# Kernel optimization log

Measured on AMD Instinct MI355X. Metric: run time of the kernel, lower is better.

The kernel has to match this reference:

```python
import jax, jax.numpy as jnp
import numpy as np

B, N, E, F = 8, 16384, 64, 64


def euler_zyx_to_matrix(J):
    # J: [..., 3] euler angles (alpha about Z, beta about Y, gamma about X)
    # R = Rz(alpha) @ Ry(beta) @ Rx(gamma)  (pytorch3d 'ZYX' convention)
    a, b, g = J[..., 0], J[..., 1], J[..., 2]
    ca, sa = jnp.cos(a), jnp.sin(a)
    cb, sb = jnp.cos(b), jnp.sin(b)
    cg, sg = jnp.cos(g), jnp.sin(g)
    r00 = ca * cb
    r01 = ca * sb * sg - sa * cg
    r02 = ca * sb * cg + sa * sg
    r10 = sa * cb
    r11 = sa * sb * sg + ca * cg
    r12 = sa * sb * cg - ca * sg
    r20 = -sb
    r21 = cb * sg
    r22 = cb * cg
    R = jnp.stack([
        jnp.stack([r00, r01, r02], axis=-1),
        jnp.stack([r10, r11, r12], axis=-1),
        jnp.stack([r20, r21, r22], axis=-1),
    ], axis=-2)  # [..., 3, 3]
    return R


def setup_inputs() -> dict:
    key = jax.random.key(0)
    k1, k2, k3, k4, k5 = jax.random.split(key, 5)
    X = jax.random.normal(k1, (B, N, E, 3), dtype=jnp.float32)
    J = jax.random.uniform(k2, (B, N, E, 3), dtype=jnp.float32)
    A = jax.random.normal(k3, (F, E), dtype=jnp.float32)
    Bw = jax.random.normal(k4, (F, E), dtype=jnp.float32)
    C = jax.random.normal(k5, (F, E), dtype=jnp.float32)
    return {"X": X, "J": J, "A": A, "Bw": Bw, "C": C}


def reference(X, J, A, Bw, C):
    R = euler_zyx_to_matrix(J)                 # [B, N, E, 3, 3]
    # v = R^T X  (per-point 3-vector): v_i = sum_k R[..., k, i] * X[..., k]
    v = jnp.einsum('bneki,bnek->bnei', R, X)   # [B, N, E, 3]
    col0 = R[..., :, 0]                        # [B, N, E, 3]
    col1 = R[..., :, 1]
    col2 = R[..., :, 2]
    v0 = v[..., 0:1]
    v1 = v[..., 1:2]
    v2 = v[..., 2:3]
    a_term = col0 * v0 + col1 * v1             # [B, N, E, 3]
    b_term = col1 * v0 - col0 * v1
    c_term = col2 * v2
    Y = (jnp.einsum('fe,bnei->bnfi', A, a_term)
         + jnp.einsum('fe,bnei->bnfi', Bw, b_term)
         + jnp.einsum('fe,bnei->bnfi', C, c_term))
    return Y
```

## Files before the change

### kernel.cpp

```cpp
#include <hip/hip_runtime.h>


#define NPOS   131072
#define PB     16
#define NC     (PB * 3)
#define ITERS  8
#define BLOCKS (NPOS / (PB * ITERS))
#define THREADS 256
#define PPW    4

typedef _Float16 half8 __attribute__((ext_vector_type(8)));
typedef float floatx4 __attribute__((ext_vector_type(4)));

__global__ __launch_bounds__(THREADS, 4)
void fused_mfma(const float* __restrict__ X, const float* __restrict__ J,
                const float* __restrict__ A, const float* __restrict__ Bw,
                const float* __restrict__ Cm, float* __restrict__ Y) {
    __shared__ _Float16 Tl[6][NC][4][8];
    __shared__ float Ys[PB * 192];

    const int lane = threadIdx.x & 63;
    const int w    = threadIdx.x >> 6;
    const int tid  = threadIdx.x;

    const int fa  = w * 16 + (lane & 15);
    const int kgA = lane >> 4;
    half8 afrag[6];
    #pragma unroll
    for (int ks = 0; ks < 6; ++ks) {
        const float* mat = (ks < 2) ? A : (ks < 4 ? Bw : Cm);
        const float* src = mat + fa * 64 + (ks & 1) * 32 + kgA * 8;
        float4 lo = *(const float4*)src;
        float4 hi = *(const float4*)(src + 4);
        half8 h;
        h[0] = (_Float16)lo.x; h[1] = (_Float16)lo.y;
        h[2] = (_Float16)lo.z; h[3] = (_Float16)lo.w;
        h[4] = (_Float16)hi.x; h[5] = (_Float16)hi.y;
        h[6] = (_Float16)hi.z; h[7] = (_Float16)hi.w;
        afrag[ks] = h;
    }

    const int ks0 = lane >> 5;
    const int kgW = (lane & 31) >> 3;
    const int jW  = lane & 7;
    const int kgR = (lane >> 4) ^ (((lane & 15) >> 1) & 3);

    float jrA[PPW][3], xrA[PPW][3], jrB[PPW][3], xrB[PPW][3];

#define LOAD_BODY(JR, XR, T)                                                  \
    {                                                                         \
        _Pragma("unroll")                                                     \
        for (int q = 0; q < PPW; ++q) {                                       \
            const int p = (blockIdx.x * ITERS + (T)) * PB + w * PPW + q;      \
            const float* jp = J + (size_t)(p * 64 + lane) * 3;                \
            const float* xp = X + (size_t)(p * 64 + lane) * 3;                \
            JR[q][0] = jp[0]; JR[q][1] = jp[1]; JR[q][2] = jp[2];             \
            XR[q][0] = xp[0]; XR[q][1] = xp[1]; XR[q][2] = xp[2];             \
        }                                                                     \
    }

#define P1_BODY(JR, XR)                                                       \
    {                                                                         \
        _Pragma("unroll")                                                     \
        for (int q = 0; q < PPW; ++q) {                                       \
            const int p_local = w * PPW + q;                                  \
            float ja = JR[q][0], jb = JR[q][1], jg = JR[q][2];                \
            float x0 = XR[q][0], x1 = XR[q][1], x2 = XR[q][2];                \
            float sa, ca, sb, cb, sg, cg;                                     \
            __sincosf(ja, &sa, &ca);                                          \
            __sincosf(jb, &sb, &cb);                                          \
            __sincosf(jg, &sg, &cg);                                          \
            float casb = ca * sb, sasb = sa * sb;                             \
            float r00 = ca * cb, r01 = casb * sg - sa * cg;                   \
            float r02 = casb * cg + sa * sg;                                  \
            float r10 = sa * cb, r11 = sasb * sg + ca * cg;                   \
            float r12 = sasb * cg - ca * sg;                                  \
            float r20 = -sb, r21 = cb * sg, r22 = cb * cg;                    \
            float v0 = fmaf(r00, x0, fmaf(r10, x1, r20 * x2));                \
            float v1 = fmaf(r01, x0, fmaf(r11, x1, r21 * x2));                \
            float v2 = fmaf(r02, x0, fmaf(r12, x1, r22 * x2));                \
            float ta[3], tb[3], tc[3];                                        \
            ta[0] = fmaf(r00, v0, r01 * v1);                                  \
            ta[1] = fmaf(r10, v0, r11 * v1);                                  \
            ta[2] = fmaf(r20, v0, r21 * v1);                                  \
            tb[0] = fmaf(r01, v0, -r00 * v1);                                 \
            tb[1] = fmaf(r11, v0, -r10 * v1);                                 \
            tb[2] = fmaf(r21, v0, -r20 * v1);                                 \
            tc[0] = r02 * v2; tc[1] = r12 * v2; tc[2] = r22 * v2;             \
            _Pragma("unroll")                                                 \
            for (int i = 0; i < 3; ++i) {                                     \
                const int n  = p_local * 3 + i;                               \
                const int kg = kgW ^ ((n >> 1) & 3);                          \
                Tl[0 + ks0][n][kg][jW] = (_Float16)ta[i];                     \
                Tl[2 + ks0][n][kg][jW] = (_Float16)tb[i];                     \
                Tl[4 + ks0][n][kg][jW] = (_Float16)tc[i];                     \
            }                                                                 \
        }                                                                     \
    }

#define P2_BODY()                                                             \
    {                                                                         \
        _Pragma("unroll")                                                     \
        for (int nt = 0; nt < 3; ++nt) {                                      \
            floatx4 acc = {0.f, 0.f, 0.f, 0.f};                               \
            _Pragma("unroll")                                                 \
            for (int ks = 0; ks < 6; ++ks) {                                  \
                half8 b = *(const half8*)&Tl[ks][nt * 16 + (lane & 15)][kgR][0]; \
                acc = __builtin_amdgcn_mfma_f32_16x16x32_f16(afrag[ks], b, acc, 0, 0, 0); \
            }                                                                 \
            const int n   = nt * 16 + (lane & 15);                            \
            const int pl2 = (n * 171) >> 9;               \
            const int i2  = n - pl2 * 3;                                      \
            const int fb  = w * 16 + (lane >> 4) * 4;                         \
            _Pragma("unroll")                                                 \
            for (int r = 0; r < 4; ++r) {                                     \
                const int z  = pl2 * 192 + (fb + r) * 3 + i2;                 \
                const int c  = z >> 2;                                        \
                const int zp = ((c ^ ((c >> 4) & 15)) << 2) | (z & 3);        \
                Ys[zp] = acc[r];                                              \
            }                                                                 \
        }                                                                     \
    }

#define STORE_BODY(T)                                                         \
    {                                                                         \
        float* yb = Y + (size_t)(blockIdx.x * ITERS + (T)) * PB * 192;        \
        _Pragma("unroll")                                                     \
        for (int k = 0; k < 3; ++k) {                                         \
            const int c  = tid + 256 * k;                                     \
            const int cp = c ^ ((c >> 4) & 15);                               \
            floatx4 v = *(const floatx4*)&Ys[cp * 4];                         \
            __builtin_nontemporal_store(v, (floatx4*)(yb + (size_t)c * 4));   \
        }                                                                     \
    }

    LOAD_BODY(jrA, xrA, 0);
    LOAD_BODY(jrB, xrB, 1);
    P1_BODY(jrA, xrA);
    for (int m = 0; m < ITERS / 2; ++m) {
        __syncthreads();
        if (m < ITERS / 2 - 1) LOAD_BODY(jrA, xrA, 2 * m + 2);
        P2_BODY();
        __syncthreads();
        STORE_BODY(2 * m);
        P1_BODY(jrB, xrB);
        __syncthreads();
        if (m < ITERS / 2 - 1) LOAD_BODY(jrB, xrB, 2 * m + 3);
        P2_BODY();
        __syncthreads();
        STORE_BODY(2 * m + 1);
        if (m < ITERS / 2 - 1) P1_BODY(jrA, xrA);
    }
#undef LOAD_BODY
#undef P1_BODY
#undef P2_BODY
#undef STORE_BODY
}

extern "C" void kernel_launch(void* const* d_in, const int* in_sizes, int n_in,
                              void* d_out, int out_size, void* d_ws, size_t ws_size,
                              hipStream_t stream) {
    const float* X  = (const float*)d_in[0];
    const float* J  = (const float*)d_in[1];
    const float* A  = (const float*)d_in[2];
    const float* Bw = (const float*)d_in[3];
    const float* Cm = (const float*)d_in[4];
    float* Y = (float*)d_out;
    fused_mfma<<<BLOCKS, THREADS, 0, stream>>>(X, J, A, Bw, Cm, Y);
}
```

Measured before the change: 53.60 us.

## Switch to persistent grid-strided scheduling with fixed grid of 1280 blocks

Replaces the fixed 8-units-per-block mapping (1024 blocks) with a 1280-block grid where each block walks units strided by the grid size, processing 6 or 7 units with a tail step. The intent is to match the grid to CU count times occupancy (256 CUs × 5) and fill all CUs evenly, reducing the partial last wave. The risk is load imbalance between blocks doing 6 versus 7 units, and more strided address patterns.

```diff
diff --git a/kernel.cpp b/kernel.cpp
--- a/kernel.cpp
+++ b/kernel.cpp
@@ -4,8 +4,8 @@
 #define NPOS   131072
 #define PB     16
 #define NC     (PB * 3)
-#define ITERS  8
-#define BLOCKS (NPOS / (PB * ITERS))
+#define NUNITS (NPOS / PB)
+#define GRID   1280
 #define THREADS 256
 #define PPW    4
 
@@ -22,6 +22,9 @@
     const int lane = threadIdx.x & 63;
     const int w    = threadIdx.x >> 6;
     const int tid  = threadIdx.x;
+    const int bid  = blockIdx.x;
+
+    const int NU = (NUNITS - bid + GRID - 1) / GRID;
 
     const int fa  = w * 16 + (lane & 15);
     const int kgA = lane >> 4;
@@ -47,11 +50,11 @@
 
     float jrA[PPW][3], xrA[PPW][3], jrB[PPW][3], xrB[PPW][3];
 
-#define LOAD_BODY(JR, XR, T)                                                  \
+#define LOAD_BODY(JR, XR, U)                                                  \
     {                                                                         \
         _Pragma("unroll")                                                     \
         for (int q = 0; q < PPW; ++q) {                                       \
-            const int p = (blockIdx.x * ITERS + (T)) * PB + w * PPW + q;      \
+            const int p = (U) * PB + w * PPW + q;                             \
             const float* jp = J + (size_t)(p * 64 + lane) * 3;                \
             const float* xp = X + (size_t)(p * 64 + lane) * 3;                \
             JR[q][0] = jp[0]; JR[q][1] = jp[1]; JR[q][2] = jp[2];             \
@@ -122,9 +125,9 @@
         }                                                                     \
     }
 
-#define STORE_BODY(T)                                                         \
+#define STORE_BODY(U)                                                         \
     {                                                                         \
-        float* yb = Y + (size_t)(blockIdx.x * ITERS + (T)) * PB * 192;        \
+        float* yb = Y + (size_t)(U) * PB * 192;                               \
         _Pragma("unroll")                                                     \
         for (int k = 0; k < 3; ++k) {                                         \
             const int c  = tid + 256 * k;                                     \
@@ -134,22 +137,30 @@
         }                                                                     \
     }
 
-    LOAD_BODY(jrA, xrA, 0);
-    LOAD_BODY(jrB, xrB, 1);
+    LOAD_BODY(jrA, xrA, bid);
+    LOAD_BODY(jrB, xrB, bid + GRID);
     P1_BODY(jrA, xrA);
-    for (int m = 0; m < ITERS / 2; ++m) {
+    #pragma unroll 1
+    for (int m = 0; m < 3; ++m) {
+        const int t0 = 2 * m;
         __syncthreads();
-        if (m < ITERS / 2 - 1) LOAD_BODY(jrA, xrA, 2 * m + 2);
+        if (t0 + 2 < NU) LOAD_BODY(jrA, xrA, bid + (t0 + 2) * GRID);
         P2_BODY();
         __syncthreads();
-        STORE_BODY(2 * m);
+        STORE_BODY(bid + t0 * GRID);
         P1_BODY(jrB, xrB);
         __syncthreads();
-        if (m < ITERS / 2 - 1) LOAD_BODY(jrB, xrB, 2 * m + 3);
+        if (t0 + 3 < NU) LOAD_BODY(jrB, xrB, bid + (t0 + 3) * GRID);
         P2_BODY();
         __syncthreads();
-        STORE_BODY(2 * m + 1);
-        if (m < ITERS / 2 - 1) P1_BODY(jrA, xrA);
+        STORE_BODY(bid + (t0 + 1) * GRID);
+        if (t0 + 2 < NU) P1_BODY(jrA, xrA);
+    }
+    if (NU == 7) {
+        __syncthreads();
+        P2_BODY();
+        __syncthreads();
+        STORE_BODY(bid + 6 * GRID);
     }
 #undef LOAD_BODY
 #undef P1_BODY
@@ -166,5 +177,5 @@
     const float* Bw = (const float*)d_in[3];
     const float* Cm = (const float*)d_in[4];
     float* Y = (float*)d_out;
-    fused_mfma<<<BLOCKS, THREADS, 0, stream>>>(X, J, A, Bw, Cm, Y);
+    fused_mfma<<<GRID, THREADS, 0, stream>>>(X, J, A, Bw, Cm, Y);
 }
```

Result: no change. 54.17 us (+1.1%).

## Store MFMA results directly to global and halve iterations per block

Applied to the files above, without the earlier changes.

Removes the LDS staging buffer for output tiles and writes each accumulator element straight to global memory with strided scalar stores, dropping the shared-memory round trip. It also halves ITERS, which doubles the number of blocks. The direct stores are scattered 4-byte writes with a stride of 3 floats, so coalescing is worse than the earlier vectorized nontemporal float4 stores. Freeing the LDS buffer may allow higher occupancy.

```diff
diff --git a/kernel.cpp b/kernel.cpp
--- a/kernel.cpp
+++ b/kernel.cpp
@@ -4,7 +4,7 @@
 #define NPOS   131072
 #define PB     16
 #define NC     (PB * 3)
-#define ITERS  8
+#define ITERS  4
 #define BLOCKS (NPOS / (PB * ITERS))
 #define THREADS 256
 #define PPW    4
@@ -17,11 +17,9 @@
                 const float* __restrict__ A, const float* __restrict__ Bw,
                 const float* __restrict__ Cm, float* __restrict__ Y) {
     __shared__ _Float16 Tl[6][NC][4][8];
-    __shared__ float Ys[PB * 192];
 
     const int lane = threadIdx.x & 63;
     const int w    = threadIdx.x >> 6;
-    const int tid  = threadIdx.x;
 
     const int fa  = w * 16 + (lane & 15);
     const int kgA = lane >> 4;
@@ -98,7 +96,7 @@
         }                                                                     \
     }
 
-#define P2_BODY()                                                             \
+#define P2_BODY(T)                                                            \
     {                                                                         \
         _Pragma("unroll")                                                     \
         for (int nt = 0; nt < 3; ++nt) {                                      \
@@ -111,26 +109,12 @@
             const int n   = nt * 16 + (lane & 15);                            \
             const int pl2 = (n * 171) >> 9;               \
             const int i2  = n - pl2 * 3;                                      \
+            const int p2  = (blockIdx.x * ITERS + (T)) * PB + pl2;            \
+            float* yp = Y + (size_t)p2 * 192 + i2;                            \
             const int fb  = w * 16 + (lane >> 4) * 4;                         \
             _Pragma("unroll")                                                 \
-            for (int r = 0; r < 4; ++r) {                                     \
-                const int z  = pl2 * 192 + (fb + r) * 3 + i2;                 \
-                const int c  = z >> 2;                                        \
-                const int zp = ((c ^ ((c >> 4) & 15)) << 2) | (z & 3);        \
-                Ys[zp] = acc[r];                                              \
-            }                                                                 \
-        }                                                                     \
-    }
-
-#define STORE_BODY(T)                                                         \
-    {                                                                         \
-        float* yb = Y + (size_t)(blockIdx.x * ITERS + (T)) * PB * 192;        \
-        _Pragma("unroll")                                                     \
-        for (int k = 0; k < 3; ++k) {                                         \
-            const int c  = tid + 256 * k;                                     \
-            const int cp = c ^ ((c >> 4) & 15);                               \
-            floatx4 v = *(const floatx4*)&Ys[cp * 4];                         \
-            __builtin_nontemporal_store(v, (floatx4*)(yb + (size_t)c * 4));   \
+            for (int r = 0; r < 4; ++r)                                       \
+                yp[(fb + r) * 3] = acc[r];                                    \
         }                                                                     \
     }
 
@@ -140,21 +124,18 @@
     for (int m = 0; m < ITERS / 2; ++m) {
         __syncthreads();
         if (m < ITERS / 2 - 1) LOAD_BODY(jrA, xrA, 2 * m + 2);
-        P2_BODY();
+        P2_BODY(2 * m);
         __syncthreads();
-        STORE_BODY(2 * m);
         P1_BODY(jrB, xrB);
         __syncthreads();
         if (m < ITERS / 2 - 1) LOAD_BODY(jrB, xrB, 2 * m + 3);
-        P2_BODY();
+        P2_BODY(2 * m + 1);
         __syncthreads();
-        STORE_BODY(2 * m + 1);
         if (m < ITERS / 2 - 1) P1_BODY(jrA, xrA);
     }
 #undef LOAD_BODY
 #undef P1_BODY
 #undef P2_BODY
-#undef STORE_BODY
 }
 
 extern "C" void kernel_launch(void* const* d_in, const int* in_sizes, int n_in,
```

Measured after the change: 92.66 us. +72.9%, slower.

## Alias LDS staging buffers and halve per-block iterations to raise occupancy

Applied to the files above, without the earlier changes.

The fp16 operand tile and the fp32 output staging buffer now share one LDS allocation, which cuts shared memory per block roughly in half. To make the aliasing safe, the MFMA phase is split into a read phase that holds three accumulators and a separate write phase, with extra barriers between them. ITERS drops from 8 to 4, which doubles the block count. The goal is more resident blocks per CU and better load balance, at the cost of more __syncthreads per iteration and extra accumulator registers.

```diff
diff --git a/kernel.cpp b/kernel.cpp
--- a/kernel.cpp
+++ b/kernel.cpp
@@ -4,7 +4,7 @@
 #define NPOS   131072
 #define PB     16
 #define NC     (PB * 3)
-#define ITERS  8
+#define ITERS  4
 #define BLOCKS (NPOS / (PB * ITERS))
 #define THREADS 256
 #define PPW    4
@@ -16,8 +16,10 @@
 void fused_mfma(const float* __restrict__ X, const float* __restrict__ J,
                 const float* __restrict__ A, const float* __restrict__ Bw,
                 const float* __restrict__ Cm, float* __restrict__ Y) {
-    __shared__ _Float16 Tl[6][NC][4][8];
-    __shared__ float Ys[PB * 192];
+    __shared__ __align__(16) char ldsbuf[6 * NC * 4 * 8 * 2];
+    _Float16* TlF = (_Float16*)ldsbuf;
+    float*    Ys  = (float*)ldsbuf;
+#define TL(ks, n, kg, j) TlF[((((ks) * NC + (n)) * 4 + (kg)) * 8 + (j))]
 
     const int lane = threadIdx.x & 63;
     const int w    = threadIdx.x >> 6;
@@ -44,8 +46,10 @@
     const int kgW = (lane & 31) >> 3;
     const int jW  = lane & 7;
     const int kgR = (lane >> 4) ^ (((lane & 15) >> 1) & 3);
+    const int nR  = lane & 15;
 
     float jrA[PPW][3], xrA[PPW][3], jrB[PPW][3], xrB[PPW][3];
+    floatx4 acc0, acc1, acc2;
 
 #define LOAD_BODY(JR, XR, T)                                                  \
     {                                                                         \
@@ -91,35 +95,49 @@
             for (int i = 0; i < 3; ++i) {                                     \
                 const int n  = p_local * 3 + i;                               \
                 const int kg = kgW ^ ((n >> 1) & 3);                          \
-                Tl[0 + ks0][n][kg][jW] = (_Float16)ta[i];                     \
-                Tl[2 + ks0][n][kg][jW] = (_Float16)tb[i];                     \
-                Tl[4 + ks0][n][kg][jW] = (_Float16)tc[i];                     \
+                TL(0 + ks0, n, kg, jW) = (_Float16)ta[i];                     \
+                TL(2 + ks0, n, kg, jW) = (_Float16)tb[i];                     \
+                TL(4 + ks0, n, kg, jW) = (_Float16)tc[i];                     \
             }                                                                 \
         }                                                                     \
     }
 
-#define P2_BODY()                                                             \
+#define P2R_BODY()                                                            \
     {                                                                         \
+        acc0 = (floatx4){0.f, 0.f, 0.f, 0.f};                                 \
+        acc1 = (floatx4){0.f, 0.f, 0.f, 0.f};                                 \
+        acc2 = (floatx4){0.f, 0.f, 0.f, 0.f};                                 \
         _Pragma("unroll")                                                     \
-        for (int nt = 0; nt < 3; ++nt) {                                      \
-            floatx4 acc = {0.f, 0.f, 0.f, 0.f};                               \
-            _Pragma("unroll")                                                 \
-            for (int ks = 0; ks < 6; ++ks) {                                  \
-                half8 b = *(const half8*)&Tl[ks][nt * 16 + (lane & 15)][kgR][0]; \
-                acc = __builtin_amdgcn_mfma_f32_16x16x32_f16(afrag[ks], b, acc, 0, 0, 0); \
-            }                                                                 \
-            const int n   = nt * 16 + (lane & 15);                            \
-            const int pl2 = (n * 171) >> 9;               \
-            const int i2  = n - pl2 * 3;                                      \
-            const int fb  = w * 16 + (lane >> 4) * 4;                         \
-            _Pragma("unroll")                                                 \
-            for (int r = 0; r < 4; ++r) {                                     \
-                const int z  = pl2 * 192 + (fb + r) * 3 + i2;                 \
-                const int c  = z >> 2;                                        \
-                const int zp = ((c ^ ((c >> 4) & 15)) << 2) | (z & 3);        \
-                Ys[zp] = acc[r];                                              \
-            }                                                                 \
+        for (int ks = 0; ks < 6; ++ks) {                                      \
+            half8 b0 = *(const half8*)&TL(ks,  0 + nR, kgR, 0);               \
+            half8 b1 = *(const half8*)&TL(ks, 16 + nR, kgR, 0);               \
+            half8 b2 = *(const half8*)&TL(ks, 32 + nR, kgR, 0);               \
+            acc0 = __builtin_amdgcn_mfma_f32_16x16x32_f16(afrag[ks], b0, acc0, 0, 0, 0); \
+            acc1 = __builtin_amdgcn_mfma_f32_16x16x32_f16(afrag[ks], b1, acc1, 0, 0, 0); \
+            acc2 = __builtin_amdgcn_mfma_f32_16x16x32_f16(afrag[ks], b2, acc2, 0, 0, 0); \
         }                                                                     \
+    }
+
+#define YS_WRITE(ACC, NT)                                                     \
+    {                                                                         \
+        const int n   = (NT) * 16 + nR;                                       \
+        const int pl2 = (n * 171) >> 9;                   \
+        const int i2  = n - pl2 * 3;                                          \
+        const int fb  = w * 16 + (lane >> 4) * 4;                             \
+        _Pragma("unroll")                                                     \
+        for (int r = 0; r < 4; ++r) {                                         \
+            const int z  = pl2 * 192 + (fb + r) * 3 + i2;                     \
+            const int c  = z >> 2;                                            \
+            const int zp = ((c ^ ((c >> 4) & 15)) << 2) | (z & 3);            \
+            Ys[zp] = ACC[r];                                                  \
+        }                                                                     \
+    }
+
+#define P2W_BODY()                                                            \
+    {                                                                         \
+        YS_WRITE(acc0, 0)                                                     \
+        YS_WRITE(acc1, 1)                                                     \
+        YS_WRITE(acc2, 2)                                                     \
     }
 
 #define STORE_BODY(T)                                                         \
@@ -140,21 +158,32 @@
     for (int m = 0; m < ITERS / 2; ++m) {
         __syncthreads();
         if (m < ITERS / 2 - 1) LOAD_BODY(jrA, xrA, 2 * m + 2);
-        P2_BODY();
+        P2R_BODY();
+        __syncthreads();
+        P2W_BODY();
         __syncthreads();
         STORE_BODY(2 * m);
+        __syncthreads();
         P1_BODY(jrB, xrB);
         __syncthreads();
         if (m < ITERS / 2 - 1) LOAD_BODY(jrB, xrB, 2 * m + 3);
-        P2_BODY();
+        P2R_BODY();
+        __syncthreads();
+        P2W_BODY();
         __syncthreads();
         STORE_BODY(2 * m + 1);
-        if (m < ITERS / 2 - 1) P1_BODY(jrA, xrA);
+        if (m < ITERS / 2 - 1) {
+            __syncthreads();
+            P1_BODY(jrA, xrA);
+        }
     }
 #undef LOAD_BODY
 #undef P1_BODY
-#undef P2_BODY
+#undef P2R_BODY
+#undef P2W_BODY
+#undef YS_WRITE
 #undef STORE_BODY
+#undef TL
 }
 
 extern "C" void kernel_launch(void* const* d_in, const int* in_sizes, int n_in,
```

After: 175.3 us. 3.27x slower.
